# Performance work log

Hardware: AMD Instinct MI355X
Metric: run time of the kernel (lower is better)

The kernel has to match this reference:

```python
import jax, jax.numpy as jnp
import numpy as np

ALPHA = 0.2      # leaky_relu negative slope
EPS = 1e-5       # BatchNorm eps
NEG = -9e15      # masked attention fill (matches -9000000000000000.0)


def _xavier(key, shape):
    fan_in, fan_out = shape[-2], shape[-1]
    lim = jnp.sqrt(6.0 / (fan_in + fan_out))
    return jax.random.uniform(key, shape, minval=-lim, maxval=lim, dtype=jnp.float32)


def setup_inputs() -> dict:
    key = jax.random.key(0)
    ks = jax.random.split(key, 10)
    b, N, L = 8, 1024, 4
    C, G, O, F = 128, 128, 64, 64   # n_feats, global_feats, global_out_feats, n_filters
    V = jax.random.normal(ks[0], (b, N, C), dtype=jnp.float32)
    A = jax.random.normal(ks[1], (b, N, L, N), dtype=jnp.float32)
    global_state = jax.random.normal(ks[2], (b, G), dtype=jnp.float32)
    graph_size = jax.random.randint(ks[3], (b,), 0, N, dtype=jnp.int32)
    subgraph_size = jax.random.randint(ks[4], (b, 1), 0, N, dtype=jnp.int32)
    Wg = _xavier(ks[5], (G, O))                 # broadcast_global_state.weights[0]
    W = _xavier(ks[6], (L, C + O, F))           # GAT per-channel weight_list
    a1 = _xavier(ks[7], (L, F, 1))
    a2 = _xavier(ks[8], (L, F, 1))
    bias_gat = jnp.full((F,), 0.01, dtype=jnp.float32)
    gamma_n = jnp.ones((F,), jnp.float32); beta_n = jnp.zeros((F,), jnp.float32)
    gamma_g = jnp.ones((O,), jnp.float32); beta_g = jnp.zeros((O,), jnp.float32)
    return dict(V=V, A=A, global_state=global_state, graph_size=graph_size,
                subgraph_size=subgraph_size, Wg=Wg, W=W, a1=a1, a2=a2,
                bias_gat=bias_gat, gamma_n=gamma_n, beta_n=beta_n,
                gamma_g=gamma_g, beta_g=beta_g)


def reference(V, A, global_state, graph_size, subgraph_size,
              Wg, W, a1, a2, bias_gat, gamma_n, beta_n, gamma_g, beta_g):
    b, N, C = V.shape
    # --- GraphNodeCatGlobalFeatures (mols=1): project global state, broadcast to
    # the first graph_size[i] nodes of each graph, zeros for padding nodes.
    gs = global_state @ Wg                                   # [b, O]
    node_mask = (jnp.arange(N)[None, :] < graph_size[:, None]).astype(V.dtype)  # [b, N]
    Vg = jnp.concatenate([V, gs[:, None, :] * node_mask[:, :, None]], axis=-1)  # [b, N, C+O]
    # --- GraphAttentionLayer, all adj channels vectorized. dropout=0.
    h = jnp.einsum('bnc,lcf->lbnf', Vg, W)                   # [L, b, N, F]
    f1 = jnp.einsum('lbnf,lf->lbn', h, a1[:, :, 0])          # [L, b, N]
    f2 = jnp.einsum('lbnf,lf->lbn', h, a2[:, :, 0])
    e = jax.nn.leaky_relu(f1[:, :, :, None] + f2[:, :, None, :], ALPHA)  # [L, b, N, N]
    adj = jnp.transpose(A, (2, 0, 1, 3))                     # [L, b, N, N]
    att = jnp.where(adj > 0, e, jnp.asarray(NEG, e.dtype))
    att = jax.nn.softmax(att, axis=2)                        # torch softmax dim=1 (row index)
    out = jnp.einsum('lbnm,lbmf->bnf', att, h) + bias_gat    # sum over channels, [b, N, F]
    # --- bn_graph (BatchNorm1d over feature channel, training-mode batch stats) + relu
    mu = out.mean(axis=(0, 1))
    var = out.var(axis=(0, 1))
    out = jax.nn.relu((out - mu) / jnp.sqrt(var + EPS) * gamma_n + beta_n)
    # --- bn_global + relu on the projected global state
    gmu = gs.mean(axis=0)
    gvar = gs.var(axis=0)
    gs_out = jax.nn.relu((gs - gmu) / jnp.sqrt(gvar + EPS) * gamma_g + beta_g)
    return (out, gs_out)
```

## Files before the change

kernel.cpp:

```cpp
#include <hip/hip_runtime.h>
#include <hip/hip_fp16.h>

typedef unsigned long long u64;
typedef unsigned short ushort_t;
typedef __attribute__((ext_vector_type(8))) short short8v;
typedef __attribute__((ext_vector_type(16))) float f32x16;

#define DI __device__ __forceinline__

DI unsigned cvt_pk_bf16(float lo, float hi) {
    unsigned r;
    asm volatile("v_cvt_pk_bf16_f32 %0, %1, %2" : "=v"(r) : "v"(lo), "v"(hi));
    return r;
}

__global__ __launch_bounds__(256)
void k_h(const float* V, const int* gsize, const float* gstate, const float* Wg,
         const float* W, const float* a1, const float* a2,
         ushort_t* hT, float* f1, float* f2)
{
    int blk = blockIdx.x;
    int b = blk >> 5, nt = blk & 31, n0 = nt * 32;
    int t = threadIdx.x;
    __shared__ float gss[64];
    __shared__ float was[2][4][192];
    __shared__ float vg[32][194];
    if (t < 64) {
        float acc = 0.f;
        for (int c = 0; c < 128; ++c) acc += gstate[b*128 + c] * Wg[c*64 + t];
        gss[t] = acc;
    } else {
        int tt = t - 64;
        #pragma unroll
        for (int k = 0; k < 8; ++k) {
            int e = tt + k*192;
            int which = (e >= 768) ? 1 : 0;
            int idx = which ? e - 768 : e;
            int l = idx / 192, c = idx - l*192;
            const float* ap = (which ? a2 : a1) + l*64;
            const float* wp = W + (l*192 + c) * 64;
            float s = 0.f;
            for (int f = 0; f < 64; ++f) s += wp[f] * ap[f];
            was[which][l][c] = s;
        }
    }
    __syncthreads();
    {
        int r = t >> 3, c0 = (t & 7) * 16;
        const float* vp = V + ((size_t)(b*1024 + n0 + r) * 128 + c0);
        float4 v0 = *(const float4*)(vp + 0);
        float4 v1 = *(const float4*)(vp + 4);
        float4 v2 = *(const float4*)(vp + 8);
        float4 v3 = *(const float4*)(vp + 12);
        *(float4*)&vg[r][c0 + 0]  = v0;
        *(float4*)&vg[r][c0 + 4]  = v1;
        *(float4*)&vg[r][c0 + 8]  = v2;
        *(float4*)&vg[r][c0 + 12] = v3;
    }
    {
        int r = t >> 3, o0 = (t & 7) * 8;
        bool on = (n0 + r) < gsize[b];
        for (int j = 0; j < 8; ++j) vg[r][128 + o0 + j] = on ? gss[o0 + j] : 0.f;
    }
    __syncthreads();
    int ty = t >> 5, tx = t & 31;
    int r0 = ty * 4;
    int j0 = tx * 8;
    int lw = j0 >> 6, f0 = j0 & 63;
    float acc[4][8];
    for (int i = 0; i < 4; ++i) for (int j = 0; j < 8; ++j) acc[i][j] = 0.f;
    const float* wp = W + (size_t)(lw*192) * 64 + f0;
    for (int c = 0; c < 192; ++c) {
        float4 wl = *(const float4*)(wp + c*64);
        float4 wh = *(const float4*)(wp + c*64 + 4);
        float wf[8] = {wl.x, wl.y, wl.z, wl.w, wh.x, wh.y, wh.z, wh.w};
        float a0 = vg[r0+0][c], a1v = vg[r0+1][c], a2v = vg[r0+2][c], a3v = vg[r0+3][c];
        for (int j = 0; j < 8; ++j) {
            acc[0][j] += a0  * wf[j];
            acc[1][j] += a1v * wf[j];
            acc[2][j] += a2v * wf[j];
            acc[3][j] += a3v * wf[j];
        }
    }
    int lb = lw*8 + b;
    #pragma unroll
    for (int j = 0; j < 8; ++j) {
        uint2 st;
        st.x = cvt_pk_bf16(acc[0][j], acc[1][j]);
        st.y = cvt_pk_bf16(acc[2][j], acc[3][j]);
        *(uint2*)(hT + ((size_t)(lb*64 + f0 + j)) * 1024 + n0 + r0) = st;
    }
    {
        int r = t & 31, l = (t >> 5) & 3, which = t >> 7;
        const float* wl = &was[which][l][0];
        float s = 0.f;
        for (int c = 0; c < 192; ++c) s += vg[r][c] * wl[c];
        float* dst = which ? f2 : f1;
        dst[(l*8 + b) * 1024 + n0 + r] = s;
    }
}

__global__ __launch_bounds__(256)
void k_maskcolsum(const float* A, const float* f1, const float* f2,
                  u64* maskp, float* psum)
{
    int blk = blockIdx.x;
    int nc = blk & 63, l = (blk >> 6) & 3, b = blk >> 8;
    int t = threadIdx.x;
    int wv = t >> 6, lane = t & 63;
    int lb = l*8 + b;
    int n0 = nc*16 + wv*4;
    ushort_t* mp16 = (ushort_t*)maskp;

    float K[16], F2[16];
    {
        const float* f2p = f2 + lb*1024 + lane*16;
        #pragma unroll
        for (int q = 0; q < 4; ++q) {
            float4 v = *(const float4*)(f2p + q*4);
            float x[4] = {v.x, v.y, v.z, v.w};
            #pragma unroll
            for (int i = 0; i < 4; ++i) {
                F2[q*4 + i] = x[i];
                K[q*4 + i]  = fmaxf(x[i], 0.2f*x[i]) + 12.f;
            }
        }
    }
    float s[16];
    #pragma unroll
    for (int j = 0; j < 16; ++j) s[j] = 0.f;

    const float* Ap = A + (((size_t)(b*1024 + n0) * 4 + l) * 1024) + lane*16;
    const float* f1p = f1 + lb*1024;
    float4 c0 = *(const float4*)(Ap + 0);
    float4 c1 = *(const float4*)(Ap + 4);
    float4 c2 = *(const float4*)(Ap + 8);
    float4 c3 = *(const float4*)(Ap + 12);
    #pragma unroll
    for (int r = 0; r < 4; ++r) {
        float va[16] = {c0.x,c0.y,c0.z,c0.w, c1.x,c1.y,c1.z,c1.w,
                        c2.x,c2.y,c2.z,c2.w, c3.x,c3.y,c3.z,c3.w};
        if (r < 3) {
            const float* An = Ap + (size_t)(r + 1) * 4096;
            c0 = *(const float4*)(An + 0);
            c1 = *(const float4*)(An + 4);
            c2 = *(const float4*)(An + 8);
            c3 = *(const float4*)(An + 12);
        }
        float f1n = f1p[n0 + r];
        unsigned bits = 0;
        #pragma unroll
        for (int j = 0; j < 16; ++j) {
            bool pos = va[j] > 0.f;
            bits |= pos ? (1u << j) : 0u;
            float x = f1n + F2[j];
            x = fmaxf(x, 0.2f * x);
            float p = __expf(x - K[j]);
            s[j] += pos ? p : 0.f;
        }
        mp16[(((size_t)(b*1024 + n0 + r) * 4 + l) << 6) + lane] = (ushort_t)bits;
    }
    __shared__ float ss[4][64][17];
    #pragma unroll
    for (int j = 0; j < 16; ++j) ss[wv][lane][j] = s[j];
    __syncthreads();
    #pragma unroll
    for (int q = 0; q < 4; ++q) {
        int m = q*256 + t;
        int l2 = m >> 4, j = m & 15;
        float v = (ss[0][l2][j] + ss[1][l2][j]) + (ss[2][l2][j] + ss[3][l2][j]);
        psum[(size_t)nc*32768 + lb*1024 + m] = v;
    }
}

__global__ __launch_bounds__(256)
void k_csum(const float* psum, const float* f2, float* ecol, float* base)
{
    int i = blockIdx.x * 256 + threadIdx.x;
    float s = 0.f;
    #pragma unroll
    for (int k = 0; k < 64; ++k) s += psum[(size_t)k*32768 + i];
    float x = f2[i];
    float K = fmaxf(x, 0.2f*x) + 12.f;
    bool emp = (s == 0.f);
    ecol[i] = emp ? 0.f : __expf(-K) / s;
    base[i] = emp ? (1.f/1024.f) : 0.f;
}

__global__ __launch_bounds__(256)
void k_pass2(const ushort_t* hT, const u64* maskp, const float* f1,
             const float* f2, const float* ecol, const float* base, __half* outl2)
{
    int blk = blockIdx.x;
    int nt = blk & 7, b = (blk >> 3) & 7, l = (blk >> 6) & 3, ks = blk >> 8;
    int lb = l*8 + b;
    int n0 = nt*128;
    int m0 = ks*512;
    int t = threadIdx.x;
    int w = t >> 6, lane = t & 63;
    int rl = lane & 31, kg = lane >> 5;

    __shared__ float f2t[512], ect[512], bat[512];
    __shared__ ushort_t hl[64][72];

    for (int k = 0; k < 2; ++k) {
        int j = t + k*256;
        f2t[j] = f2[lb*1024 + m0 + j];
        ect[j] = ecol[lb*1024 + m0 + j];
        bat[j] = base[lb*1024 + m0 + j];
    }
    int nrow = n0 + w*32 + rl;
    float f1v = f1[lb*1024 + nrow];
    const u64* mrow = maskp + ((size_t)(b*1024 + nrow)*4 + l)*16 + ks*8;

    f32x16 acc0 = {0,0,0,0,0,0,0,0,0,0,0,0,0,0,0,0};
    f32x16 acc1 = {0,0,0,0,0,0,0,0,0,0,0,0,0,0,0,0};

    int hf = t >> 2, hseg = t & 3;
    const ushort_t* hsrc = hT + ((size_t)(lb*64 + hf)) * 1024 + m0 + hseg*16;

    for (int kc = 0; kc < 8; ++kc) {
        __syncthreads();
        {
            const uint4* s = (const uint4*)(hsrc + kc*64);
            uint4 q0 = s[0], q1 = s[1];
            *(uint4*)&hl[hf][hseg*16]     = q0;
            *(uint4*)&hl[hf][hseg*16 + 8] = q1;
        }
        u64 wm = mrow[kc];
        __syncthreads();
        #pragma unroll
        for (int kk = 0; kk < 4; ++kk) {
            int jb = kc*64 + kk*16 + kg*8;
            float4 fa = *(float4*)&f2t[jb];
            float4 fb = *(float4*)&f2t[jb+4];
            float4 ea = *(float4*)&ect[jb];
            float4 eb = *(float4*)&ect[jb+4];
            float4 ba = *(float4*)&bat[jb];
            float4 bb = *(float4*)&bat[jb+4];
            unsigned mb = (unsigned)(wm >> (kk*16 + kg*8)) & 0xffu;
            float xs[8] = {fa.x,fa.y,fa.z,fa.w,fb.x,fb.y,fb.z,fb.w};
            float es[8] = {ea.x,ea.y,ea.z,ea.w,eb.x,eb.y,eb.z,eb.w};
            float bs[8] = {ba.x,ba.y,ba.z,ba.w,bb.x,bb.y,bb.z,bb.w};
            float av[8];
            #pragma unroll
            for (int i = 0; i < 8; ++i) {
                float x = f1v + xs[i];
                x = fmaxf(x, 0.2f * x);
                float p = __expf(x) * es[i];
                av[i] = (mb & (1u << i)) ? p : bs[i];
            }
            union { unsigned u[4]; short8v s; } af;
            af.u[0] = cvt_pk_bf16(av[0], av[1]);
            af.u[1] = cvt_pk_bf16(av[2], av[3]);
            af.u[2] = cvt_pk_bf16(av[4], av[5]);
            af.u[3] = cvt_pk_bf16(av[6], av[7]);
            short8v b0 = *(short8v*)&hl[rl][kk*16 + kg*8];
            short8v b1 = *(short8v*)&hl[32 + rl][kk*16 + kg*8];
            acc0 = __builtin_amdgcn_mfma_f32_32x32x16_bf16(af.s, b0, acc0, 0, 0, 0);
            acc1 = __builtin_amdgcn_mfma_f32_32x32x16_bf16(af.s, b1, acc1, 0, 0, 0);
        }
    }
    int sl = ks*4 + l;
    __half* op = outl2 + ((size_t)(sl*8 + b) * 1024) * 64;
    #pragma unroll
    for (int r = 0; r < 16; ++r) {
        int row = n0 + w*32 + (r & 3) + 8*(r >> 2) + 4*kg;
        op[(size_t)row*64 + rl]      = __float2half(acc0[r]);
        op[(size_t)row*64 + 32 + rl] = __float2half(acc1[r]);
    }
}

__global__ __launch_bounds__(256)
void k_reduce(const __half* outl2, const float* bias, float* outpre, float* bnsum, float* bnsumsq)
{
    int blk = blockIdx.x, t = threadIdx.x;
    __shared__ float red[2][64];
    if (t < 128) red[t >> 6][t & 63] = 0.f;
    __syncthreads();
    size_t idx = (size_t)blk * 2048 + t * 8;
    int fb = (t * 8) & 63;
    float o[8];
    for (int j = 0; j < 8; ++j) o[j] = bias[fb + j];
    #pragma unroll
    for (int sl = 0; sl < 8; ++sl) {
        uint4 u = *(const uint4*)(outl2 + (size_t)sl * 524288 + idx);
        const __half* hh = (const __half*)&u;
        #pragma unroll
        for (int j = 0; j < 8; ++j) o[j] += __half2float(hh[j]);
    }
    *(float4*)(outpre + idx)     = make_float4(o[0], o[1], o[2], o[3]);
    *(float4*)(outpre + idx + 4) = make_float4(o[4], o[5], o[6], o[7]);
    for (int j = 0; j < 8; ++j) {
        atomicAdd(&red[0][fb + j], o[j]);
        atomicAdd(&red[1][fb + j], o[j]*o[j]);
    }
    __syncthreads();
    if (t < 64) { atomicAdd(&bnsum[t], red[0][t]); atomicAdd(&bnsumsq[t], red[1][t]); }
}

__global__ __launch_bounds__(256)
void k_bnapply(const float* outpre, const float* bnsum, const float* bnsumsq,
               const float* gamma, const float* beta, float* out,
               const float* gstate, const float* Wg,
               const float* gamma_g, const float* beta_g, float* out_gs)
{
    int blk = blockIdx.x, t = threadIdx.x;
    __shared__ float gsa[512];
    __shared__ float gmu[64], grs[64];
    if (blk == 0) {
        for (int p = t; p < 512; p += 256) {
            int bb = p >> 6, o = p & 63;
            float acc = 0.f;
            for (int c = 0; c < 128; ++c) acc += gstate[bb*128 + c] * Wg[c*64 + o];
            gsa[p] = acc;
        }
        __syncthreads();
        if (t < 64) {
            float s = 0.f, sq = 0.f;
            for (int bb = 0; bb < 8; ++bb) { float v = gsa[bb*64 + t]; s += v; sq += v*v; }
            float mu = s * 0.125f;
            float var = sq * 0.125f - mu*mu;
            gmu[t] = mu; grs[t] = rsqrtf(var + 1e-5f);
        }
        __syncthreads();
        for (int p = t; p < 512; p += 256) {
            int o = p & 63;
            float v = (gsa[p] - gmu[o]) * grs[o] * gamma_g[o] + beta_g[o];
            out_gs[p] = fmaxf(v, 0.f);
        }
    }
    int f0 = (t * 4) & 63;
    float mu[4], rstd[4], ga[4], be[4];
    for (int j = 0; j < 4; ++j) {
        float sm = bnsum[f0 + j], sq = bnsumsq[f0 + j];
        float m = sm * (1.f / 8192.f);
        float var = sq * (1.f / 8192.f) - m*m;
        mu[j] = m; rstd[j] = rsqrtf(var + 1e-5f);
        ga[j] = gamma[f0 + j]; be[j] = beta[f0 + j];
    }
    for (int g = 0; g < 4; ++g) {
        size_t base = (size_t)blk * 4096 + g * 1024 + t * 4;
        float4 v = *(const float4*)(outpre + base);
        float x[4] = {v.x, v.y, v.z, v.w};
        float y[4];
        for (int j = 0; j < 4; ++j) {
            float z = (x[j] - mu[j]) * rstd[j] * ga[j] + be[j];
            y[j] = fmaxf(z, 0.f);
        }
        *(float4*)(out + base) = make_float4(y[0], y[1], y[2], y[3]);
    }
}

extern "C" void kernel_launch(void* const* d_in, const int* in_sizes, int n_in,
                              void* d_out, int out_size, void* d_ws, size_t ws_size,
                              hipStream_t stream)
{
    const float* V       = (const float*)d_in[0];
    const float* A       = (const float*)d_in[1];
    const float* gstate  = (const float*)d_in[2];
    const int*   gsize   = (const int*)d_in[3];
    const float* Wg      = (const float*)d_in[5];
    const float* W       = (const float*)d_in[6];
    const float* a1      = (const float*)d_in[7];
    const float* a2      = (const float*)d_in[8];
    const float* bias    = (const float*)d_in[9];
    const float* gamma_n = (const float*)d_in[10];
    const float* beta_n  = (const float*)d_in[11];
    const float* gamma_g = (const float*)d_in[12];
    const float* beta_g  = (const float*)d_in[13];

    char* ws = (char*)d_ws;
    float*    f1      = (float*)(ws + 0);
    float*    f2      = (float*)(ws + 131072);
    float*    ecol    = (float*)(ws + 262144);
    float*    base    = (float*)(ws + 393216);
    float*    bnsum   = (float*)(ws + 524288);
    float*    bnsumsq = (float*)(ws + 524544);
    u64*      maskp   = (u64*)  (ws + 525312);
    ushort_t* hT      = (ushort_t*)(ws + 4719616);
    float*    psum    = (float*)(ws + 8913920);
    __half*   outl2   = (__half*)(ws + 17302528);
    float*    outpre  = (float*)(ws + 25691136);

    float* out_main = (float*)d_out;
    float* out_gs   = out_main + 524288;

    (void)hipMemsetAsync(bnsum, 0, 512, stream);
    hipLaunchKernelGGL(k_h,          dim3(256),  dim3(256), 0, stream,
                       V, gsize, gstate, Wg, W, a1, a2, hT, f1, f2);
    hipLaunchKernelGGL(k_maskcolsum, dim3(2048), dim3(256), 0, stream,
                       A, f1, f2, maskp, psum);
    hipLaunchKernelGGL(k_csum,       dim3(128),  dim3(256), 0, stream,
                       psum, f2, ecol, base);
    hipLaunchKernelGGL(k_pass2,      dim3(512),  dim3(256), 0, stream,
                       hT, maskp, f1, f2, ecol, base, outl2);
    hipLaunchKernelGGL(k_reduce,     dim3(256),  dim3(256), 0, stream,
                       outl2, bias, outpre, bnsum, bnsumsq);
    hipLaunchKernelGGL(k_bnapply,    dim3(128),  dim3(256), 0, stream,
                       outpre, bnsum, bnsumsq, gamma_n, beta_n, out_main,
                       gstate, Wg, gamma_g, beta_g, out_gs);
}
```

Baseline: 129.8 us.

## Coarsen mask/colsum blocks to 16 rows per wave with double-buffered A loads

k_maskcolsum now processes 16 rows per wave instead of 4, using a quarter as many blocks. A rows are loaded in batches of four through two register buffers so loads overlap compute, and f1 values are preloaded with vector loads. The partial-sum buffer shrinks from 64 to 16 chunks, which lightens k_csum's reduction and compacts the workspace layout. In exchange register pressure rises, with launch bounds requesting 2 blocks per SIMD, and the grid now has fewer blocks to hide latency on the bandwidth-bound A stream.

```diff
diff --git a/kernel.cpp b/kernel.cpp
--- a/kernel.cpp
+++ b/kernel.cpp
@@ -100,66 +100,92 @@
     }
 }
 
-__global__ __launch_bounds__(256)
+__global__ __launch_bounds__(256, 2)
 void k_maskcolsum(const float* A, const float* f1, const float* f2,
                   u64* maskp, float* psum)
 {
     int blk = blockIdx.x;
-    int nc = blk & 63, l = (blk >> 6) & 3, b = blk >> 8;
+    int nc = blk & 15, l = (blk >> 4) & 3, b = blk >> 6;
     int t = threadIdx.x;
     int wv = t >> 6, lane = t & 63;
     int lb = l*8 + b;
-    int n0 = nc*16 + wv*4;
+    int n0 = nc*64 + wv*16;
     ushort_t* mp16 = (ushort_t*)maskp;
 
-    float K[16], F2[16];
+    float K[16], F2r[16];
     {
         const float* f2p = f2 + lb*1024 + lane*16;
         #pragma unroll
         for (int q = 0; q < 4; ++q) {
             float4 v = *(const float4*)(f2p + q*4);
-            float x[4] = {v.x, v.y, v.z, v.w};
+            float x4[4] = {v.x, v.y, v.z, v.w};
             #pragma unroll
             for (int i = 0; i < 4; ++i) {
-                F2[q*4 + i] = x[i];
-                K[q*4 + i]  = fmaxf(x[i], 0.2f*x[i]) + 12.f;
+                F2r[q*4 + i] = x4[i];
+                K[q*4 + i]   = fmaxf(x4[i], 0.2f*x4[i]) + 12.f;
             }
         }
     }
+    float f1r[16];
+    {
+        const float* f1p = f1 + lb*1024 + n0;
+        #pragma unroll
+        for (int q = 0; q < 4; ++q) {
+            float4 v = *(const float4*)(f1p + q*4);
+            f1r[q*4+0] = v.x; f1r[q*4+1] = v.y; f1r[q*4+2] = v.z; f1r[q*4+3] = v.w;
+        }
+    }
     float s[16];
     #pragma unroll
     for (int j = 0; j < 16; ++j) s[j] = 0.f;
 
-    const float* Ap = A + (((size_t)(b*1024 + n0) * 4 + l) * 1024) + lane*16;
-    const float* f1p = f1 + lb*1024;
-    float4 c0 = *(const float4*)(Ap + 0);
-    float4 c1 = *(const float4*)(Ap + 4);
-    float4 c2 = *(const float4*)(Ap + 8);
-    float4 c3 = *(const float4*)(Ap + 12);
-    #pragma unroll
-    for (int r = 0; r < 4; ++r) {
-        float va[16] = {c0.x,c0.y,c0.z,c0.w, c1.x,c1.y,c1.z,c1.w,
-                        c2.x,c2.y,c2.z,c2.w, c3.x,c3.y,c3.z,c3.w};
-        if (r < 3) {
-            const float* An = Ap + (size_t)(r + 1) * 4096;
-            c0 = *(const float4*)(An + 0);
-            c1 = *(const float4*)(An + 4);
-            c2 = *(const float4*)(An + 8);
-            c3 = *(const float4*)(An + 12);
-        }
-        float f1n = f1p[n0 + r];
-        unsigned bits = 0;
-        #pragma unroll
-        for (int j = 0; j < 16; ++j) {
-            bool pos = va[j] > 0.f;
-            bits |= pos ? (1u << j) : 0u;
-            float x = f1n + F2[j];
-            x = fmaxf(x, 0.2f * x);
-            float p = __expf(x - K[j]);
-            s[j] += pos ? p : 0.f;
-        }
-        mp16[(((size_t)(b*1024 + n0 + r) * 4 + l) << 6) + lane] = (ushort_t)bits;
-    }
+    const float* Abase = A + (((size_t)(b*1024 + n0) * 4 + l) * 1024) + lane*16;
+
+    auto LOADB = [&](float4* dst, int batch) {
+        #pragma unroll
+        for (int r = 0; r < 4; ++r) {
+            const float* ap = Abase + (size_t)(batch*4 + r) * 4096;
+            dst[r*4+0] = *(const float4*)(ap + 0);
+            dst[r*4+1] = *(const float4*)(ap + 4);
+            dst[r*4+2] = *(const float4*)(ap + 8);
+            dst[r*4+3] = *(const float4*)(ap + 12);
+        }
+    };
+    auto PROC = [&](float4* src, int batch) {
+        #pragma unroll
+        for (int r = 0; r < 4; ++r) {
+            int n = n0 + batch*4 + r;
+            float f1n = f1r[batch*4 + r];
+            unsigned bits = 0;
+            #pragma unroll
+            for (int q = 0; q < 4; ++q) {
+                float4 v = src[r*4 + q];
+                float x4[4] = {v.x, v.y, v.z, v.w};
+                #pragma unroll
+                for (int i = 0; i < 4; ++i) {
+                    int j = q*4 + i;
+                    bool pos = x4[i] > 0.f;
+                    bits |= pos ? (1u << j) : 0u;
+                    float x = f1n + F2r[j];
+                    x = fmaxf(x, 0.2f * x);
+                    float p = __expf(x - K[j]);
+                    s[j] += pos ? p : 0.f;
+                }
+            }
+            mp16[(((size_t)(b*1024 + n) * 4 + l) << 6) + lane] = (ushort_t)bits;
+        }
+    };
+
+    float4 Abuf[16], Bbuf[16];
+    LOADB(Abuf, 0);
+    LOADB(Bbuf, 1);
+    PROC(Abuf, 0);
+    LOADB(Abuf, 2);
+    PROC(Bbuf, 1);
+    LOADB(Bbuf, 3);
+    PROC(Abuf, 2);
+    PROC(Bbuf, 3);
+
     __shared__ float ss[4][64][17];
     #pragma unroll
     for (int j = 0; j < 16; ++j) ss[wv][lane][j] = s[j];
@@ -179,7 +205,7 @@
     int i = blockIdx.x * 256 + threadIdx.x;
     float s = 0.f;
     #pragma unroll
-    for (int k = 0; k < 64; ++k) s += psum[(size_t)k*32768 + i];
+    for (int k = 0; k < 16; ++k) s += psum[(size_t)k*32768 + i];
     float x = f2[i];
     float K = fmaxf(x, 0.2f*x) + 12.f;
     bool emp = (s == 0.f);
@@ -380,8 +406,8 @@
     u64*      maskp   = (u64*)  (ws + 525312);
     ushort_t* hT      = (ushort_t*)(ws + 4719616);
     float*    psum    = (float*)(ws + 8913920);
-    __half*   outl2   = (__half*)(ws + 17302528);
-    float*    outpre  = (float*)(ws + 25691136);
+    __half*   outl2   = (__half*)(ws + 11011072);
+    float*    outpre  = (float*)(ws + 19399680);
 
     float* out_main = (float*)d_out;
     float* out_gs   = out_main + 524288;
@@ -389,7 +415,7 @@
     (void)hipMemsetAsync(bnsum, 0, 512, stream);
     hipLaunchKernelGGL(k_h,          dim3(256),  dim3(256), 0, stream,
                        V, gsize, gstate, Wg, W, a1, a2, hT, f1, f2);
-    hipLaunchKernelGGL(k_maskcolsum, dim3(2048), dim3(256), 0, stream,
+    hipLaunchKernelGGL(k_maskcolsum, dim3(512),  dim3(256), 0, stream,
                        A, f1, f2, maskp, psum);
     hipLaunchKernelGGL(k_csum,       dim3(128),  dim3(256), 0, stream,
                        psum, f2, ecol, base);
```

After: 136.8 us. +5.3%, slower.
